# Performance work log

Hardware: AMD Instinct MI355X
Metric: run time of the kernel (lower is better)

The kernel has to match this reference:

```python
import jax, jax.numpy as jnp
import numpy as np

N_NODES = 131072
N_DST = 16384        # batch_size * num_supernodes = 8 * 2048
DEG = 16
N_EDGES = N_DST * DEG
IN_DIM, HID, NDIM = 3, 256, 2
POS_STD = 1.0


def _linear_params(key, fan_in, fan_out):
    # xavier_uniform weights, zero bias; torch Linear stores W as [out, in]
    limit = np.sqrt(6.0 / (fan_in + fan_out)).astype(np.float32)
    w = jax.random.uniform(key, (fan_out, fan_in), jnp.float32, -limit, limit)
    return w, jnp.zeros((fan_out,), jnp.float32)


def setup_inputs() -> dict:
    key = jax.random.key(0)
    ks = jax.random.split(key, 12)
    x = jax.random.normal(ks[0], (N_NODES, IN_DIM), jnp.float32)
    mesh_pos = jax.random.uniform(ks[1], (N_NODES, NDIM), jnp.float32)
    # dst column sorted, each supernode id 0..N_DST-1 appears DEG times (segment_csr layout)
    dst = jnp.repeat(jnp.arange(N_DST, dtype=jnp.int64), DEG)
    src = jax.random.randint(ks[2], (N_EDGES,), 0, N_NODES, jnp.int64)
    mesh_edges = jnp.stack([dst, src], axis=1)  # [E, 2] = (dst, src)
    batch_idx = jnp.repeat(jnp.arange(8, dtype=jnp.int64), N_NODES // 8)
    ip_w1, ip_b1 = _linear_params(ks[3], IN_DIM, HID)
    ip_w2, ip_b2 = _linear_params(ks[4], HID, HID)
    ip_w3, ip_b3 = _linear_params(ks[5], HID, HID)
    msg_w1, msg_b1 = _linear_params(ks[6], 2 * HID, 2 * HID)
    msg_w2, msg_b2 = _linear_params(ks[7], 2 * HID, HID)
    msg_w3, msg_b3 = _linear_params(ks[8], HID, HID)
    b_fourier = jax.random.normal(ks[9], (HID // 2, NDIM), jnp.float32) * POS_STD
    return {
        "x": x, "mesh_pos": mesh_pos, "mesh_edges": mesh_edges, "batch_idx": batch_idx,
        "ip_w1": ip_w1, "ip_b1": ip_b1, "ip_w2": ip_w2, "ip_b2": ip_b2,
        "ip_w3": ip_w3, "ip_b3": ip_b3, "b_fourier": b_fourier,
        "msg_w1": msg_w1, "msg_b1": msg_b1, "msg_w2": msg_w2, "msg_b2": msg_b2,
        "msg_w3": msg_w3, "msg_b3": msg_b3,
        "batch_size": 8, "num_supernodes": 2048,
    }


def reference(x, mesh_pos, mesh_edges, batch_idx,
              ip_w1, ip_b1, ip_w2, ip_b2, ip_w3, ip_b3, b_fourier,
              msg_w1, msg_b1, msg_w2, msg_b2, msg_w3, msg_b3,
              batch_size, num_supernodes):
    gelu = lambda t: jax.nn.gelu(t, approximate=False)  # torch nn.GELU default (erf)
    # input_proj MLP
    h = gelu(x @ ip_w1.T + ip_b1)
    h = gelu(h @ ip_w2.T + ip_b2)
    h = h @ ip_w3.T + ip_b3
    # gaussian sincos positional embedding
    proj = (2.0 * jnp.pi) * (mesh_pos @ b_fourier.T)  # [N, HID/2]
    h = h + jnp.concatenate([jnp.cos(proj), jnp.sin(proj)], axis=-1)
    # edge gather + concat + message MLP
    dst, src = mesh_edges[:, 0], mesh_edges[:, 1]
    m = jnp.concatenate([h[src], h[dst]], axis=1)  # [E, 2*HID]
    m = gelu(m @ msg_w1.T + msg_b1)
    m = gelu(m @ msg_w2.T + msg_b2)
    m = m @ msg_w3.T + msg_b3
    # segment mean over (sorted, compact) destination supernodes
    num_dst = batch_size * num_supernodes
    sums = jax.ops.segment_sum(m, dst, num_segments=num_dst)
    counts = jax.ops.segment_sum(jnp.ones((dst.shape[0],), m.dtype), dst, num_segments=num_dst)
    out = sums / jnp.maximum(counts, 1.0)[:, None]
    return out.reshape(batch_size, num_supernodes, out.shape[-1])
```

## Files before the change

### kernel.cpp

```cpp
#include <hip/hip_runtime.h>
#include <math.h>

#define N_NODES 131072
#define N_DST   16384
#define DEG     16
#define HID     256
#define N_EDGES 262144

typedef __bf16 bf16_8 __attribute__((ext_vector_type(8)));
typedef float  f32_4  __attribute__((ext_vector_type(4)));

__device__ __forceinline__ float gelu_f(float v) {
    float u = fmaf(v * v, -0.10294324f, -2.30220819f) * v;
    float e;
    asm("v_exp_f32 %0, %1" : "=v"(e) : "v"(u));
    return v * __builtin_amdgcn_rcpf(1.0f + e);
}
__device__ __forceinline__ f32_4 zero4() {
    f32_4 z; z[0] = 0.f; z[1] = 0.f; z[2] = 0.f; z[3] = 0.f; return z;
}

__device__ __forceinline__ void load_lds16(const __bf16* g, __bf16* l) {
    __builtin_amdgcn_global_load_lds(
        (__attribute__((address_space(1))) void*)g,
        (__attribute__((address_space(3))) void*)l, 16, 0, 0);
}

__global__ void prep_kernel(__bf16* __restrict__ out,
                            const float* __restrict__ w2,
                            const float* __restrict__ w3,
                            const float* __restrict__ mw1,
                            const float* __restrict__ mw2,
                            const float* __restrict__ mw3) {
    int stride = gridDim.x * blockDim.x;
    for (int i = blockIdx.x * blockDim.x + threadIdx.x; i < 589824; i += stride) {
        float v;
        if      (i <  65536) v = w2[i];
        else if (i < 131072) v = w3[i - 65536];
        else if (i < 393216) v = mw1[i - 131072];
        else if (i < 524288) v = mw2[i - 393216];
        else                 v = mw3[i - 524288];
        out[i] = (__bf16)v;
    }
}

__global__ __launch_bounds__(256) void enc1_kernel(
    const float* __restrict__ x, const float* __restrict__ w1,
    const float* __restrict__ b1, __bf16* __restrict__ h1) {
    const int c8   = threadIdx.x & 31;
    const int nloc = threadIdx.x >> 5;
    float w[24], bb[8];
    #pragma unroll
    for (int i = 0; i < 6; i++) *(float4*)&w[i * 4] = ((const float4*)w1)[c8 * 6 + i];
    *(float4*)&bb[0] = ((const float4*)b1)[c8 * 2 + 0];
    *(float4*)&bb[4] = ((const float4*)b1)[c8 * 2 + 1];
    for (int n = blockIdx.x * 8 + nloc; n < N_NODES; n += gridDim.x * 8) {
        float x0 = x[n * 3 + 0], x1 = x[n * 3 + 1], x2 = x[n * 3 + 2];
        bf16_8 o;
        #pragma unroll
        for (int j = 0; j < 8; j++) {
            float v = fmaf(x2, w[j * 3 + 2],
                      fmaf(x1, w[j * 3 + 1],
                      fmaf(x0, w[j * 3 + 0], bb[j])));
            o[j] = (__bf16)gelu_f(v);
        }
        *(bf16_8*)&h1[(size_t)n * 256 + c8 * 8] = o;
    }
}

__global__ __launch_bounds__(256, 2) void enc23_kernel(
    __bf16* __restrict__ hA,
    const __bf16* __restrict__ W2, const float* __restrict__ b2,
    const __bf16* __restrict__ W3, const float* __restrict__ b3,
    const float* __restrict__ pos, const float* __restrict__ bfour)
{
    __shared__ __align__(16) __bf16 sA[64 * 64];
    __shared__ __align__(16) __bf16 sB[16384];
    __shared__ __align__(16) __bf16 sH2[64 * 256];

    const int tid = threadIdx.x;
    const int m0  = blockIdx.x * 64;
    const int wave = tid >> 6, lane = tid & 63, ln = lane & 15, quad = lane >> 4;
    const int wm = wave >> 1, wn = wave & 1;

    const __bf16* pA[2];
    #pragma unroll
    for (int i = 0; i < 2; i++) {
        int idx = i * 256 + tid;
        int row = idx >> 3, kg = (idx & 7) ^ (row & 7);
        pA[i] = hA + (size_t)(m0 + row) * 256 + kg * 8;
    }

    f32_4 acc[2][8];
    #pragma unroll
    for (int i = 0; i < 2; i++)
        #pragma unroll
        for (int j = 0; j < 8; j++) acc[i][j] = zero4();

    bf16_8 ar[2];
    #pragma unroll
    for (int i = 0; i < 2; i++) ar[i] = *(const bf16_8*)pA[i];

    #pragma unroll
    for (int kb = 0; kb < 4; kb++) {
        if (kb > 0) __syncthreads();
        #pragma unroll
        for (int i = 0; i < 2; i++)
            *(bf16_8*)&sA[(i * 256 + tid) * 8] = ar[i];
        #pragma unroll
        for (int i = 0; i < 8; i++) {
            int idx = i * 256 + tid;
            int row = idx >> 3, kg = (idx & 7) ^ (row & 7);
            load_lds16(W2 + (size_t)row * 256 + kb * 64 + kg * 8, &sB[idx * 8]);
        }
        __syncthreads();
        if (kb < 3) {
            #pragma unroll
            for (int i = 0; i < 2; i++)
                ar[i] = *(const bf16_8*)(pA[i] + (kb + 1) * 64);
        }
        #pragma unroll
        for (int ks = 0; ks < 2; ks++) {
            int c = ks * 4 + quad;
            bf16_8 af[2], bfr[8];
            #pragma unroll
            for (int mt = 0; mt < 2; mt++) {
                int mr = wm * 32 + mt * 16 + ln;
                af[mt] = *(const bf16_8*)&sA[mr * 64 + (c ^ (mr & 7)) * 8];
            }
            #pragma unroll
            for (int nt = 0; nt < 8; nt++) {
                int nr = wn * 128 + nt * 16 + ln;
                bfr[nt] = *(const bf16_8*)&sB[nr * 64 + (c ^ (nr & 7)) * 8];
            }
            #pragma unroll
            for (int mt = 0; mt < 2; mt++)
                #pragma unroll
                for (int nt = 0; nt < 8; nt++)
                    acc[mt][nt] = __builtin_amdgcn_mfma_f32_16x16x32_bf16(af[mt], bfr[nt], acc[mt][nt], 0, 0, 0);
        }
    }
    #pragma unroll
    for (int nt = 0; nt < 8; nt++) {
        int col = wn * 128 + nt * 16 + ln;
        float bb = b2[col];
        #pragma unroll
        for (int mt = 0; mt < 2; mt++) {
            #pragma unroll
            for (int r = 0; r < 4; r++) {
                int row = wm * 32 + mt * 16 + quad * 4 + r;
                sH2[row * 256 + ((col + row * 8) & 255)] = (__bf16)gelu_f(acc[mt][nt][r] + bb);
            }
        }
    }
    #pragma unroll
    for (int i = 0; i < 2; i++)
        #pragma unroll
        for (int j = 0; j < 8; j++) acc[i][j] = zero4();
    __syncthreads();

    #pragma unroll
    for (int kb = 0; kb < 4; kb++) {
        if (kb > 0) __syncthreads();
        #pragma unroll
        for (int i = 0; i < 8; i++) {
            int idx = i * 256 + tid;
            int row = idx >> 3, kg = (idx & 7) ^ (row & 7);
            load_lds16(W3 + (size_t)row * 256 + kb * 64 + kg * 8, &sB[idx * 8]);
        }
        __syncthreads();
        #pragma unroll
        for (int ks = 0; ks < 2; ks++) {
            int c = ks * 4 + quad;
            int k0 = kb * 64 + ks * 32 + quad * 8;
            bf16_8 af[2], bfr[8];
            #pragma unroll
            for (int mt = 0; mt < 2; mt++) {
                int mr = wm * 32 + mt * 16 + ln;
                af[mt] = *(const bf16_8*)&sH2[mr * 256 + ((k0 + mr * 8) & 255)];
            }
            #pragma unroll
            for (int nt = 0; nt < 8; nt++) {
                int nr = wn * 128 + nt * 16 + ln;
                bfr[nt] = *(const bf16_8*)&sB[nr * 64 + (c ^ (nr & 7)) * 8];
            }
            #pragma unroll
            for (int mt = 0; mt < 2; mt++)
                #pragma unroll
                for (int nt = 0; nt < 8; nt++)
                    acc[mt][nt] = __builtin_amdgcn_mfma_f32_16x16x32_bf16(af[mt], bfr[nt], acc[mt][nt], 0, 0, 0);
        }
    }
    __syncthreads();
    __bf16* buf = sB + wave * 4096;
    float b3r[8], Bc0[8], Bc1[8];
    #pragma unroll
    for (int nt = 0; nt < 8; nt++) {
        int col = wn * 128 + nt * 16 + ln;
        b3r[nt] = b3[col];
        int jm = col & 127;
        Bc0[nt] = bfour[jm * 2 + 0];
        Bc1[nt] = bfour[jm * 2 + 1];
    }
    const bool iscos = (wn == 0);
    #pragma unroll
    for (int mt = 0; mt < 2; mt++) {
        #pragma unroll
        for (int r = 0; r < 4; r++) {
            int rowL = mt * 16 + quad * 4 + r;
            int rowE = m0 + wm * 32 + rowL;
            float p0 = pos[rowE * 2 + 0], p1 = pos[rowE * 2 + 1];
            #pragma unroll
            for (int nt = 0; nt < 8; nt++) {
                float f = 6.2831853071795864f * fmaf(p1, Bc1[nt], p0 * Bc0[nt]);
                float v = acc[mt][nt][r] + b3r[nt] + (iscos ? __cosf(f) : __sinf(f));
                int colL = nt * 16 + ln;
                buf[rowL * 128 + ((colL + rowL * 8) & 127)] = (__bf16)v;
            }
        }
    }
    #pragma unroll
    for (int p = 0; p < 8; p++) {
        int rowL = p * 4 + (lane >> 4);
        int c8 = lane & 15;
        bf16_8 vv = *(const bf16_8*)&buf[rowL * 128 + ((c8 * 8 + rowL * 8) & 127)];
        *(bf16_8*)&hA[(size_t)(m0 + wm * 32 + rowL) * 256 + wn * 128 + c8 * 8] = vv;
    }
}

__global__ __launch_bounds__(256, 2) void msg_fused(
    const __bf16* __restrict__ h, const int* __restrict__ edges,
    const __bf16* __restrict__ W1a, const float* __restrict__ b1,
    const __bf16* __restrict__ dmat, const __bf16* __restrict__ W2,
    const float* __restrict__ b2, __bf16* __restrict__ p2)
{
    __shared__ __align__(16) __bf16 sH[64 * 256];
    __shared__ __align__(16) __bf16 sB[16384];
    __shared__ __align__(16) __bf16 sM1[64 * 128];

    const int tid = threadIdx.x;
    const int e0  = blockIdx.x * 64;
    const int wave = tid >> 6, lane = tid & 63, ln = lane & 15, quad = lane >> 4;
    const int wm = wave >> 1, wn = wave & 1;

    int* s_src = (int*)sB;
    if (tid < 64) s_src[tid] = edges[2 * (e0 + tid) + 1];
    __syncthreads();

    const __bf16* pH[8];
    #pragma unroll
    for (int i = 0; i < 8; i++) {
        int idx = i * 256 + tid;
        int row = idx >> 5, kg = (idx & 31) ^ (row & 7);
        pH[i] = h + (size_t)s_src[row] * 256 + kg * 8;
    }
    __syncthreads();
    #pragma unroll
    for (int i = 0; i < 8; i++)
        load_lds16(pH[i], &sH[(i * 256 + tid) * 8]);

    f32_4 acc2[2][8];
    #pragma unroll
    for (int i = 0; i < 2; i++)
        #pragma unroll
        for (int j = 0; j < 8; j++) acc2[i][j] = zero4();

    #pragma unroll 1
    for (int q = 0; q < 4; q++) {
        const int colbase = q * 128 + wn * 64;
        float b1r[4];
        float dr[2][4];
        #pragma unroll
        for (int nt = 0; nt < 4; nt++) {
            b1r[nt] = b1[colbase + nt * 16 + ln];
            #pragma unroll
            for (int mt = 0; mt < 2; mt++) {
                int gid = blockIdx.x * 4 + wm * 2 + mt;
                dr[mt][nt] = (float)dmat[(size_t)gid * 512 + colbase + nt * 16 + ln];
            }
        }
        f32_4 acc1[2][4];
        #pragma unroll
        for (int i = 0; i < 2; i++)
            #pragma unroll
            for (int j = 0; j < 4; j++) acc1[i][j] = zero4();

        #pragma unroll
        for (int kb = 0; kb < 2; kb++) {
            __syncthreads();
            #pragma unroll
            for (int i = 0; i < 8; i++) {
                int idx = i * 256 + tid;
                int row = idx >> 4, kg = (idx & 15) ^ (row & 7);
                load_lds16(W1a + (size_t)(q * 128 + row) * 512 + kb * 128 + kg * 8,
                           &sB[idx * 8]);
            }
            __syncthreads();
            #pragma unroll
            for (int ks = 0; ks < 4; ks++) {
                int ca = kb * 16 + ks * 4 + quad;
                int cb = ks * 4 + quad;
                bf16_8 af[2], bfr[4];
                #pragma unroll
                for (int mt = 0; mt < 2; mt++) {
                    int mr = wm * 32 + mt * 16 + ln;
                    af[mt] = *(const bf16_8*)&sH[mr * 256 + (ca ^ (mr & 7)) * 8];
                }
                #pragma unroll
                for (int nt = 0; nt < 4; nt++) {
                    int nr = wn * 64 + nt * 16 + ln;
                    bfr[nt] = *(const bf16_8*)&sB[nr * 128 + (cb ^ (nr & 7)) * 8];
                }
                #pragma unroll
                for (int mt = 0; mt < 2; mt++)
                    #pragma unroll
                    for (int nt = 0; nt < 4; nt++)
                        acc1[mt][nt] = __builtin_amdgcn_mfma_f32_16x16x32_bf16(af[mt], bfr[nt], acc1[mt][nt], 0, 0, 0);
            }
        }
        #pragma unroll
        for (int mt = 0; mt < 2; mt++) {
            #pragma unroll
            for (int nt = 0; nt < 4; nt++) {
                #pragma unroll
                for (int r = 0; r < 4; r++) {
                    int row = wm * 32 + mt * 16 + quad * 4 + r;
                    int colq = wn * 64 + nt * 16 + ln;
                    float v = gelu_f(acc1[mt][nt][r] + b1r[nt] + dr[mt][nt]);
                    sM1[row * 128 + ((colq + row * 8) & 127)] = (__bf16)v;
                }
            }
        }
        __syncthreads();

        #pragma unroll
        for (int kb2 = 0; kb2 < 2; kb2++) {
            if (kb2 > 0) __syncthreads();
            #pragma unroll
            for (int i = 0; i < 8; i++) {
                int idx = i * 256 + tid;
                int row = idx >> 3, kg = (idx & 7) ^ (row & 7);
                load_lds16(W2 + (size_t)row * 512 + q * 128 + kb2 * 64 + kg * 8,
                           &sB[idx * 8]);
            }
            __syncthreads();
            #pragma unroll
            for (int ks = 0; ks < 2; ks++) {
                int k0 = kb2 * 64 + ks * 32 + quad * 8;
                int cb2 = ks * 4 + quad;
                bf16_8 af[2], bfr[8];
                #pragma unroll
                for (int mt = 0; mt < 2; mt++) {
                    int mr = wm * 32 + mt * 16 + ln;
                    af[mt] = *(const bf16_8*)&sM1[mr * 128 + ((k0 + mr * 8) & 127)];
                }
                #pragma unroll
                for (int nt = 0; nt < 8; nt++) {
                    int nr = wn * 128 + nt * 16 + ln;
                    bfr[nt] = *(const bf16_8*)&sB[nr * 64 + (cb2 ^ (nr & 7)) * 8];
                }
                #pragma unroll
                for (int mt = 0; mt < 2; mt++)
                    #pragma unroll
                    for (int nt = 0; nt < 8; nt++)
                        acc2[mt][nt] = __builtin_amdgcn_mfma_f32_16x16x32_bf16(af[mt], bfr[nt], acc2[mt][nt], 0, 0, 0);
            }
        }
        __syncthreads();
    }

    #pragma unroll
    for (int nt = 0; nt < 8; nt++) {
        int col = wn * 128 + nt * 16 + ln;
        float bb = b2[col];
        #pragma unroll
        for (int mt = 0; mt < 2; mt++) {
            float s = gelu_f(acc2[mt][nt][0] + bb) + gelu_f(acc2[mt][nt][1] + bb)
                    + gelu_f(acc2[mt][nt][2] + bb) + gelu_f(acc2[mt][nt][3] + bb);
            s += __shfl_xor(s, 16);
            s += __shfl_xor(s, 32);
            if (quad == 0) {
                int dstn = edges[2 * (e0 + (wm * 2 + mt) * 16)];
                p2[(size_t)dstn * HID + col] = (__bf16)(s * 0.0625f);
            }
        }
    }
}

template<int K, int GMODE, int WLD, int WOFF, bool BIAS, bool POOL_, bool F32OUT>
__global__ __launch_bounds__(256, 3) void mgemm(
    const __bf16* __restrict__ Ag, const __bf16* __restrict__ h,
    const int* __restrict__ edges, const __bf16* __restrict__ W,
    const float* __restrict__ bias, __bf16* __restrict__ Cb,
    float* __restrict__ Cf, int NB, int Nfull, int e0)
{
    __shared__ __align__(16) __bf16 sA[128 * 64];
    __shared__ __align__(16) __bf16 sB[128 * 64];
    __shared__ int s_idx[128];

    const int tid  = threadIdx.x;
    const int mblk = blockIdx.x / NB;
    const int nblk = blockIdx.x % NB;
    const int m0 = mblk * 128, n0 = nblk * 128;
    const int wave = tid >> 6, lane = tid & 63, ln = lane & 15, quad = lane >> 4;
    const int wm = wave >> 1, wn = wave & 1;

    if (GMODE) {
        if (tid < 128) {
            int r = m0 + tid;
            s_idx[tid] = (GMODE == 1) ? edges[2 * (e0 + r) + 1]
                                      : edges[2 * (DEG * r)];
        }
        __syncthreads();
    }

    const __bf16* pA[4];
    const __bf16* pB[4];
    #pragma unroll
    for (int i = 0; i < 4; i++) {
        int idx = i * 256 + tid;
        int row = idx >> 3, kg = (idx & 7) ^ (row & 7);
        pA[i] = GMODE ? h + (size_t)s_idx[row] * HID + kg * 8
                      : Ag + (size_t)(m0 + row) * K + kg * 8;
        pB[i] = W + (size_t)(n0 + row) * WLD + WOFF + kg * 8;
    }
    const int ach = quad ^ (ln & 7);
    const int aof[2] = { (wm * 64 + ln) * 64 + ach * 8, (wm * 64 + ln) * 64 + (ach ^ 4) * 8 };
    const int bof[2] = { (wn * 64 + ln) * 64 + ach * 8, (wn * 64 + ln) * 64 + (ach ^ 4) * 8 };

    f32_4 acc[4][4];
    #pragma unroll
    for (int i = 0; i < 4; i++)
        #pragma unroll
        for (int j = 0; j < 4; j++) acc[i][j] = zero4();

    bf16_8 ar[4], br[4];
    #pragma unroll
    for (int i = 0; i < 4; i++) {
        ar[i] = *(const bf16_8*)pA[i];
        br[i] = *(const bf16_8*)pB[i];
    }

    #pragma unroll
    for (int kb = 0; kb < K / 64; kb++) {
        if (kb > 0) __syncthreads();
        #pragma unroll
        for (int i = 0; i < 4; i++) {
            int idx = i * 256 + tid;
            *(bf16_8*)&sA[idx * 8] = ar[i];
            *(bf16_8*)&sB[idx * 8] = br[i];
        }
        __syncthreads();
        if (kb + 1 < K / 64) {
            #pragma unroll
            for (int i = 0; i < 4; i++) {
                ar[i] = *(const bf16_8*)(pA[i] + (kb + 1) * 64);
                br[i] = *(const bf16_8*)(pB[i] + (kb + 1) * 64);
            }
        }
        #pragma unroll
        for (int ks = 0; ks < 2; ks++) {
            bf16_8 af[4], bfr[4];
            #pragma unroll
            for (int mt = 0; mt < 4; mt++) af[mt]  = *(const bf16_8*)&sA[aof[ks] + mt * 1024];
            #pragma unroll
            for (int nt = 0; nt < 4; nt++) bfr[nt] = *(const bf16_8*)&sB[bof[ks] + nt * 1024];
            #pragma unroll
            for (int mt = 0; mt < 4; mt++)
                #pragma unroll
                for (int nt = 0; nt < 4; nt++)
                    acc[mt][nt] = __builtin_amdgcn_mfma_f32_16x16x32_bf16(af[mt], bfr[nt], acc[mt][nt], 0, 0, 0);
        }
    }

    if (POOL_) {
        #pragma unroll
        for (int nt = 0; nt < 4; nt++) {
            int col = n0 + wn * 64 + nt * 16 + ln;
            float bb = BIAS ? bias[col] : 0.f;
            #pragma unroll
            for (int mt = 0; mt < 4; mt++) {
                float s = gelu_f(acc[mt][nt][0] + bb) + gelu_f(acc[mt][nt][1] + bb)
                        + gelu_f(acc[mt][nt][2] + bb) + gelu_f(acc[mt][nt][3] + bb);
                s += __shfl_xor(s, 16);
                s += __shfl_xor(s, 32);
                if (quad == 0) {
                    int eg  = e0 + m0 + wm * 64 + mt * 16;
                    int dstn = edges[2 * eg];
                    Cb[(size_t)dstn * HID + col] = (__bf16)(s * 0.0625f);
                }
            }
        }
    } else if (F32OUT) {
        #pragma unroll
        for (int nt = 0; nt < 4; nt++) {
            int col = n0 + wn * 64 + nt * 16 + ln;
            float bb = BIAS ? bias[col] : 0.f;
            #pragma unroll
            for (int mt = 0; mt < 4; mt++) {
                #pragma unroll
                for (int r = 0; r < 4; r++) {
                    int rowE = m0 + wm * 64 + mt * 16 + quad * 4 + r;
                    Cf[(size_t)rowE * Nfull + col] = acc[mt][nt][r] + bb;
                }
            }
        }
    } else {
        __syncthreads();
        __bf16* sw = ((wave & 2) ? sB : sA) + (wave & 1) * 4096;
        #pragma unroll
        for (int nt = 0; nt < 4; nt++) {
            #pragma unroll
            for (int mt = 0; mt < 4; mt++) {
                #pragma unroll
                for (int r = 0; r < 4; r++) {
                    int rowL = mt * 16 + quad * 4 + r;
                    int colL = nt * 16 + ln;
                    sw[rowL * 64 + ((colL + rowL * 8) & 63)] = (__bf16)acc[mt][nt][r];
                }
            }
        }
        __syncthreads();
        #pragma unroll
        for (int p = 0; p < 8; p++) {
            int rowL = p * 8 + (lane >> 3);
            int c8 = lane & 7;
            bf16_8 vv = *(const bf16_8*)&sw[rowL * 64 + ((c8 * 8 + rowL * 8) & 63)];
            int rowE = m0 + wm * 64 + rowL;
            *(bf16_8*)&Cb[(size_t)rowE * Nfull + n0 + wn * 64 + c8 * 8] = vv;
        }
    }
}

extern "C" void kernel_launch(void* const* d_in, const int* in_sizes, int n_in,
                              void* d_out, int out_size, void* d_ws, size_t ws_size,
                              hipStream_t stream) {
    const float* x     = (const float*)d_in[0];
    const float* pos   = (const float*)d_in[1];
    const int*   edges = (const int*)d_in[2];
    const float* ip_w1 = (const float*)d_in[4];
    const float* ip_b1 = (const float*)d_in[5];
    const float* ip_w2 = (const float*)d_in[6];
    const float* ip_b2 = (const float*)d_in[7];
    const float* ip_w3 = (const float*)d_in[8];
    const float* ip_b3 = (const float*)d_in[9];
    const float* bfour = (const float*)d_in[10];
    const float* mw1   = (const float*)d_in[11];
    const float* mb1   = (const float*)d_in[12];
    const float* mw2   = (const float*)d_in[13];
    const float* mb2   = (const float*)d_in[14];
    const float* mw3   = (const float*)d_in[15];
    const float* mb3   = (const float*)d_in[16];

    char* ws = (char*)d_ws;
    __bf16* hA = (__bf16*)ws;
    size_t off = (size_t)N_NODES * HID * 2;
    __bf16* wb = (__bf16*)(ws + off);
    off += (size_t)589824 * 2;
    off = (off + 255) & ~(size_t)255;
    __bf16* dbuf = (__bf16*)(ws + off);
    off += (size_t)N_DST * 512 * 2;
    __bf16* p2 = (__bf16*)(ws + off);
    off += (size_t)N_DST * HID * 2;

    __bf16* w2b  = wb;
    __bf16* w3b  = wb + 65536;
    __bf16* mw1b = wb + 131072;
    __bf16* mw2b = wb + 393216;
    __bf16* mw3b = wb + 524288;

    prep_kernel<<<2304, 256, 0, stream>>>(wb, ip_w2, ip_w3, mw1, mw2, mw3);

    enc1_kernel<<<2048, 256, 0, stream>>>(x, ip_w1, ip_b1, hA);
    enc23_kernel<<<2048, 256, 0, stream>>>(hA, w2b, ip_b2, w3b, ip_b3, pos, bfour);

    mgemm<256, 2, 512, 256, false, false, false><<<512, 256, 0, stream>>>(
        nullptr, hA, edges, mw1b, nullptr, dbuf, nullptr, 4, 512, 0);

    msg_fused<<<4096, 256, 0, stream>>>(hA, edges, mw1b, mb1, dbuf, mw2b, mb2, p2);

    mgemm<256, 0, 256, 0, true, false, true><<<256, 256, 0, stream>>>(
        p2, nullptr, nullptr, mw3b, mb3, nullptr, (float*)d_out, 2, 256, 0);
}
```

Baseline: 438.6 us.

## Double-buffer weight tiles, keep gathered rows in registers, use 128-edge blocks

msg_fused now runs 512 threads per block over 128 edges, so each loaded weight tile serves twice as many rows. The gathered h rows go straight from global memory into per-wave registers instead of through LDS. Weight tiles are double-buffered in LDS, with the next tile's async load issued before the current tile's MFMAs, so load latency overlaps compute and fewer barriers are needed. The cost is higher register pressure (64 extra VGPRs per thread for the A fragments), which under launch_bounds(512,2) may cause spills or lower occupancy.

```diff
diff --git a/kernel.cpp b/kernel.cpp
--- a/kernel.cpp
+++ b/kernel.cpp
@@ -228,54 +228,73 @@
     }
 }
 
-__global__ __launch_bounds__(256, 2) void msg_fused(
+__global__ __launch_bounds__(512, 2) void msg_fused(
     const __bf16* __restrict__ h, const int* __restrict__ edges,
     const __bf16* __restrict__ W1a, const float* __restrict__ b1,
     const __bf16* __restrict__ dmat, const __bf16* __restrict__ W2,
     const float* __restrict__ b2, __bf16* __restrict__ p2)
 {
-    __shared__ __align__(16) __bf16 sH[64 * 256];
-    __shared__ __align__(16) __bf16 sB[16384];
-    __shared__ __align__(16) __bf16 sM1[64 * 128];
+    __shared__ __align__(16) __bf16 sB[2][16384];
+    __shared__ __align__(16) __bf16 sM1[16384];
 
     const int tid = threadIdx.x;
-    const int e0  = blockIdx.x * 64;
+    const int e0  = blockIdx.x * 128;
     const int wave = tid >> 6, lane = tid & 63, ln = lane & 15, quad = lane >> 4;
     const int wm = wave >> 1, wn = wave & 1;
 
-    int* s_src = (int*)sB;
-    if (tid < 64) s_src[tid] = edges[2 * (e0 + tid) + 1];
+    bf16_8 aA[2][8];
+    #pragma unroll
+    for (int mt = 0; mt < 2; mt++) {
+        int row = wm * 32 + mt * 16 + ln;
+        int src = edges[2 * (e0 + row) + 1];
+        const __bf16* base = h + (size_t)src * 256 + quad * 8;
+        #pragma unroll
+        for (int c = 0; c < 8; c++)
+            aA[mt][c] = *(const bf16_8*)(base + c * 32);
+    }
+
+    int w1e[4], w2e[4];
+    #pragma unroll
+    for (int i = 0; i < 4; i++) {
+        int idx = i * 512 + tid;
+        int r1 = idx >> 4, k1 = (idx & 15) ^ (r1 & 7);
+        w1e[i] = r1 * 512 + k1 * 8;
+        int r2 = idx >> 3, k2 = (idx & 7) ^ (r2 & 7);
+        w2e[i] = r2 * 512 + k2 * 8;
+    }
+
+    auto stage_w1 = [&](int q, int kb, int p) {
+        const __bf16* srcb = W1a + (size_t)q * 128 * 512 + kb * 128;
+        #pragma unroll
+        for (int i = 0; i < 4; i++)
+            load_lds16(srcb + w1e[i], &sB[p][(i * 512 + tid) * 8]);
+    };
+    auto stage_w2 = [&](int q, int kb2, int p) {
+        const __bf16* srcb = W2 + q * 128 + kb2 * 64;
+        #pragma unroll
+        for (int i = 0; i < 4; i++)
+            load_lds16(srcb + w2e[i], &sB[p][(i * 512 + tid) * 8]);
+    };
+
+    f32_4 acc2[2][8];
+    #pragma unroll
+    for (int i = 0; i < 2; i++)
+        #pragma unroll
+        for (int j = 0; j < 8; j++) acc2[i][j] = zero4();
+
+    stage_w1(0, 0, 0);
     __syncthreads();
-
-    const __bf16* pH[8];
-    #pragma unroll
-    for (int i = 0; i < 8; i++) {
-        int idx = i * 256 + tid;
-        int row = idx >> 5, kg = (idx & 31) ^ (row & 7);
-        pH[i] = h + (size_t)s_src[row] * 256 + kg * 8;
-    }
-    __syncthreads();
-    #pragma unroll
-    for (int i = 0; i < 8; i++)
-        load_lds16(pH[i], &sH[(i * 256 + tid) * 8]);
-
-    f32_4 acc2[2][8];
-    #pragma unroll
-    for (int i = 0; i < 2; i++)
-        #pragma unroll
-        for (int j = 0; j < 8; j++) acc2[i][j] = zero4();
 
     #pragma unroll 1
     for (int q = 0; q < 4; q++) {
         const int colbase = q * 128 + wn * 64;
-        float b1r[4];
-        float dr[2][4];
+        float b1r[4], dr[2][4];
         #pragma unroll
         for (int nt = 0; nt < 4; nt++) {
             b1r[nt] = b1[colbase + nt * 16 + ln];
             #pragma unroll
             for (int mt = 0; mt < 2; mt++) {
-                int gid = blockIdx.x * 4 + wm * 2 + mt;
+                int gid = blockIdx.x * 8 + wm * 2 + mt;
                 dr[mt][nt] = (float)dmat[(size_t)gid * 512 + colbase + nt * 16 + ln];
             }
         }
@@ -285,38 +304,37 @@
             #pragma unroll
             for (int j = 0; j < 4; j++) acc1[i][j] = zero4();
 
-        #pragma unroll
-        for (int kb = 0; kb < 2; kb++) {
-            __syncthreads();
-            #pragma unroll
-            for (int i = 0; i < 8; i++) {
-                int idx = i * 256 + tid;
-                int row = idx >> 4, kg = (idx & 15) ^ (row & 7);
-                load_lds16(W1a + (size_t)(q * 128 + row) * 512 + kb * 128 + kg * 8,
-                           &sB[idx * 8]);
-            }
-            __syncthreads();
-            #pragma unroll
-            for (int ks = 0; ks < 4; ks++) {
-                int ca = kb * 16 + ks * 4 + quad;
-                int cb = ks * 4 + quad;
-                bf16_8 af[2], bfr[4];
-                #pragma unroll
-                for (int mt = 0; mt < 2; mt++) {
-                    int mr = wm * 32 + mt * 16 + ln;
-                    af[mt] = *(const bf16_8*)&sH[mr * 256 + (ca ^ (mr & 7)) * 8];
-                }
-                #pragma unroll
-                for (int nt = 0; nt < 4; nt++) {
-                    int nr = wn * 64 + nt * 16 + ln;
-                    bfr[nt] = *(const bf16_8*)&sB[nr * 128 + (cb ^ (nr & 7)) * 8];
-                }
-                #pragma unroll
-                for (int mt = 0; mt < 2; mt++)
-                    #pragma unroll
-                    for (int nt = 0; nt < 4; nt++)
-                        acc1[mt][nt] = __builtin_amdgcn_mfma_f32_16x16x32_bf16(af[mt], bfr[nt], acc1[mt][nt], 0, 0, 0);
-            }
+        stage_w1(q, 1, 1);
+        #pragma unroll
+        for (int ks = 0; ks < 4; ks++) {
+            bf16_8 bfr[4];
+            #pragma unroll
+            for (int nt = 0; nt < 4; nt++) {
+                int nr = wn * 64 + nt * 16 + ln;
+                bfr[nt] = *(const bf16_8*)&sB[0][nr * 128 + (((ks * 4 + quad) ^ (nr & 7)) * 8)];
+            }
+            #pragma unroll
+            for (int mt = 0; mt < 2; mt++)
+                #pragma unroll
+                for (int nt = 0; nt < 4; nt++)
+                    acc1[mt][nt] = __builtin_amdgcn_mfma_f32_16x16x32_bf16(aA[mt][ks], bfr[nt], acc1[mt][nt], 0, 0, 0);
+        }
+        __syncthreads();
+
+        stage_w2(q, 0, 0);
+        #pragma unroll
+        for (int ks = 0; ks < 4; ks++) {
+            bf16_8 bfr[4];
+            #pragma unroll
+            for (int nt = 0; nt < 4; nt++) {
+                int nr = wn * 64 + nt * 16 + ln;
+                bfr[nt] = *(const bf16_8*)&sB[1][nr * 128 + (((ks * 4 + quad) ^ (nr & 7)) * 8)];
+            }
+            #pragma unroll
+            for (int mt = 0; mt < 2; mt++)
+                #pragma unroll
+                for (int nt = 0; nt < 4; nt++)
+                    acc1[mt][nt] = __builtin_amdgcn_mfma_f32_16x16x32_bf16(aA[mt][4 + ks], bfr[nt], acc1[mt][nt], 0, 0, 0);
         }
         #pragma unroll
         for (int mt = 0; mt < 2; mt++) {
@@ -333,38 +351,49 @@
         }
         __syncthreads();
 
-        #pragma unroll
-        for (int kb2 = 0; kb2 < 2; kb2++) {
-            if (kb2 > 0) __syncthreads();
-            #pragma unroll
-            for (int i = 0; i < 8; i++) {
-                int idx = i * 256 + tid;
-                int row = idx >> 3, kg = (idx & 7) ^ (row & 7);
-                load_lds16(W2 + (size_t)row * 512 + q * 128 + kb2 * 64 + kg * 8,
-                           &sB[idx * 8]);
-            }
-            __syncthreads();
-            #pragma unroll
-            for (int ks = 0; ks < 2; ks++) {
-                int k0 = kb2 * 64 + ks * 32 + quad * 8;
-                int cb2 = ks * 4 + quad;
-                bf16_8 af[2], bfr[8];
-                #pragma unroll
-                for (int mt = 0; mt < 2; mt++) {
-                    int mr = wm * 32 + mt * 16 + ln;
-                    af[mt] = *(const bf16_8*)&sM1[mr * 128 + ((k0 + mr * 8) & 127)];
-                }
-                #pragma unroll
-                for (int nt = 0; nt < 8; nt++) {
-                    int nr = wn * 128 + nt * 16 + ln;
-                    bfr[nt] = *(const bf16_8*)&sB[nr * 64 + (cb2 ^ (nr & 7)) * 8];
-                }
-                #pragma unroll
-                for (int mt = 0; mt < 2; mt++)
-                    #pragma unroll
-                    for (int nt = 0; nt < 8; nt++)
-                        acc2[mt][nt] = __builtin_amdgcn_mfma_f32_16x16x32_bf16(af[mt], bfr[nt], acc2[mt][nt], 0, 0, 0);
-            }
+        stage_w2(q, 1, 1);
+        #pragma unroll
+        for (int ks = 0; ks < 2; ks++) {
+            int k0 = ks * 32 + quad * 8;
+            bf16_8 af[2], bfr[8];
+            #pragma unroll
+            for (int mt = 0; mt < 2; mt++) {
+                int mr = wm * 32 + mt * 16 + ln;
+                af[mt] = *(const bf16_8*)&sM1[mr * 128 + ((k0 + mr * 8) & 127)];
+            }
+            #pragma unroll
+            for (int nt = 0; nt < 8; nt++) {
+                int nr = wn * 128 + nt * 16 + ln;
+                bfr[nt] = *(const bf16_8*)&sB[0][nr * 64 + (((ks * 4 + quad) ^ (nr & 7)) * 8)];
+            }
+            #pragma unroll
+            for (int mt = 0; mt < 2; mt++)
+                #pragma unroll
+                for (int nt = 0; nt < 8; nt++)
+                    acc2[mt][nt] = __builtin_amdgcn_mfma_f32_16x16x32_bf16(af[mt], bfr[nt], acc2[mt][nt], 0, 0, 0);
+        }
+        __syncthreads();
+
+        if (q < 3) stage_w1(q + 1, 0, 0);
+        #pragma unroll
+        for (int ks = 0; ks < 2; ks++) {
+            int k0 = 64 + ks * 32 + quad * 8;
+            bf16_8 af[2], bfr[8];
+            #pragma unroll
+            for (int mt = 0; mt < 2; mt++) {
+                int mr = wm * 32 + mt * 16 + ln;
+                af[mt] = *(const bf16_8*)&sM1[mr * 128 + ((k0 + mr * 8) & 127)];
+            }
+            #pragma unroll
+            for (int nt = 0; nt < 8; nt++) {
+                int nr = wn * 128 + nt * 16 + ln;
+                bfr[nt] = *(const bf16_8*)&sB[1][nr * 64 + (((ks * 4 + quad) ^ (nr & 7)) * 8)];
+            }
+            #pragma unroll
+            for (int mt = 0; mt < 2; mt++)
+                #pragma unroll
+                for (int nt = 0; nt < 8; nt++)
+                    acc2[mt][nt] = __builtin_amdgcn_mfma_f32_16x16x32_bf16(af[mt], bfr[nt], acc2[mt][nt], 0, 0, 0);
         }
         __syncthreads();
     }
@@ -577,7 +606,7 @@
     mgemm<256, 2, 512, 256, false, false, false><<<512, 256, 0, stream>>>(
         nullptr, hA, edges, mw1b, nullptr, dbuf, nullptr, 4, 512, 0);
 
-    msg_fused<<<4096, 256, 0, stream>>>(hA, edges, mw1b, mb1, dbuf, mw2b, mb2, p2);
+    msg_fused<<<2048, 512, 0, stream>>>(hA, edges, mw1b, mb1, dbuf, mw2b, mb2, p2);
 
     mgemm<256, 0, 256, 0, true, false, true><<<256, 256, 0, stream>>>(
         p2, nullptr, nullptr, mw3b, mb3, nullptr, (float*)d_out, 2, 256, 0);
```

New measurement: 448.7 us. 1.02x slower.

## Precompute per-node first message-layer projection and gather it per edge

Applied to the files above, without the earlier changes.

The source half of the first message linear layer is now computed once per node by a separate GEMM into a new 512-wide bf16 buffer. The fused message kernel gathers those projected rows per edge, adds the per-destination term, and applies GELU before the second layer. The first-layer bias moves into the destination GEMM epilogue. This halves the first-layer matrix FLOPs and frees LDS so the kernel can run at occupancy 3, but it writes a large node-level intermediate and doubles the bytes gathered per edge.

```diff
diff --git a/kernel.cpp b/kernel.cpp
--- a/kernel.cpp
+++ b/kernel.cpp
@@ -228,37 +228,23 @@
     }
 }
 
-__global__ __launch_bounds__(256, 2) void msg_fused(
-    const __bf16* __restrict__ h, const int* __restrict__ edges,
-    const __bf16* __restrict__ W1a, const float* __restrict__ b1,
+__global__ __launch_bounds__(256, 3) void msg_fused(
+    const __bf16* __restrict__ an, const int* __restrict__ edges,
     const __bf16* __restrict__ dmat, const __bf16* __restrict__ W2,
     const float* __restrict__ b2, __bf16* __restrict__ p2)
 {
-    __shared__ __align__(16) __bf16 sH[64 * 256];
+    __shared__ __align__(16) __bf16 sM1[8192];
     __shared__ __align__(16) __bf16 sB[16384];
-    __shared__ __align__(16) __bf16 sM1[64 * 128];
+    __shared__ int s_src[64];
 
     const int tid = threadIdx.x;
     const int e0  = blockIdx.x * 64;
     const int wave = tid >> 6, lane = tid & 63, ln = lane & 15, quad = lane >> 4;
     const int wm = wave >> 1, wn = wave & 1;
 
-    int* s_src = (int*)sB;
     if (tid < 64) s_src[tid] = edges[2 * (e0 + tid) + 1];
     __syncthreads();
 
-    const __bf16* pH[8];
-    #pragma unroll
-    for (int i = 0; i < 8; i++) {
-        int idx = i * 256 + tid;
-        int row = idx >> 5, kg = (idx & 31) ^ (row & 7);
-        pH[i] = h + (size_t)s_src[row] * 256 + kg * 8;
-    }
-    __syncthreads();
-    #pragma unroll
-    for (int i = 0; i < 8; i++)
-        load_lds16(pH[i], &sH[(i * 256 + tid) * 8]);
-
     f32_4 acc2[2][8];
     #pragma unroll
     for (int i = 0; i < 2; i++)
@@ -267,75 +253,31 @@
 
     #pragma unroll 1
     for (int q = 0; q < 4; q++) {
-        const int colbase = q * 128 + wn * 64;
-        float b1r[4];
-        float dr[2][4];
-        #pragma unroll
-        for (int nt = 0; nt < 4; nt++) {
-            b1r[nt] = b1[colbase + nt * 16 + ln];
-            #pragma unroll
-            for (int mt = 0; mt < 2; mt++) {
-                int gid = blockIdx.x * 4 + wm * 2 + mt;
-                dr[mt][nt] = (float)dmat[(size_t)gid * 512 + colbase + nt * 16 + ln];
-            }
-        }
-        f32_4 acc1[2][4];
-        #pragma unroll
-        for (int i = 0; i < 2; i++)
-            #pragma unroll
-            for (int j = 0; j < 4; j++) acc1[i][j] = zero4();
-
-        #pragma unroll
-        for (int kb = 0; kb < 2; kb++) {
-            __syncthreads();
-            #pragma unroll
-            for (int i = 0; i < 8; i++) {
-                int idx = i * 256 + tid;
-                int row = idx >> 4, kg = (idx & 15) ^ (row & 7);
-                load_lds16(W1a + (size_t)(q * 128 + row) * 512 + kb * 128 + kg * 8,
-                           &sB[idx * 8]);
-            }
-            __syncthreads();
-            #pragma unroll
-            for (int ks = 0; ks < 4; ks++) {
-                int ca = kb * 16 + ks * 4 + quad;
-                int cb = ks * 4 + quad;
-                bf16_8 af[2], bfr[4];
-                #pragma unroll
-                for (int mt = 0; mt < 2; mt++) {
-                    int mr = wm * 32 + mt * 16 + ln;
-                    af[mt] = *(const bf16_8*)&sH[mr * 256 + (ca ^ (mr & 7)) * 8];
-                }
-                #pragma unroll
-                for (int nt = 0; nt < 4; nt++) {
-                    int nr = wn * 64 + nt * 16 + ln;
-                    bfr[nt] = *(const bf16_8*)&sB[nr * 128 + (cb ^ (nr & 7)) * 8];
-                }
-                #pragma unroll
-                for (int mt = 0; mt < 2; mt++)
-                    #pragma unroll
-                    for (int nt = 0; nt < 4; nt++)
-                        acc1[mt][nt] = __builtin_amdgcn_mfma_f32_16x16x32_bf16(af[mt], bfr[nt], acc1[mt][nt], 0, 0, 0);
-            }
-        }
-        #pragma unroll
-        for (int mt = 0; mt < 2; mt++) {
-            #pragma unroll
-            for (int nt = 0; nt < 4; nt++) {
-                #pragma unroll
-                for (int r = 0; r < 4; r++) {
-                    int row = wm * 32 + mt * 16 + quad * 4 + r;
-                    int colq = wn * 64 + nt * 16 + ln;
-                    float v = gelu_f(acc1[mt][nt][r] + b1r[nt] + dr[mt][nt]);
-                    sM1[row * 128 + ((colq + row * 8) & 127)] = (__bf16)v;
-                }
-            }
-        }
-        __syncthreads();
+        #pragma unroll
+        for (int i = 0; i < 4; i++) {
+            int idx = i * 256 + tid;
+            int row = idx >> 4, kgl = idx & 15, kg = kgl ^ (row & 7);
+            load_lds16(an + (size_t)s_src[row] * 512 + q * 128 + kg * 8,
+                       &sM1[idx * 8]);
+        }
+        __syncthreads();
+
+        #pragma unroll
+        for (int i = 0; i < 4; i++) {
+            int idx = i * 256 + tid;
+            int row = idx >> 4, kgl = idx & 15, kg = kgl ^ (row & 7);
+            int gid = blockIdx.x * 4 + (row >> 4);
+            bf16_8 a = *(const bf16_8*)&sM1[idx * 8];
+            bf16_8 d = *(const bf16_8*)&dmat[(size_t)gid * 512 + q * 128 + kg * 8];
+            bf16_8 o;
+            #pragma unroll
+            for (int j = 0; j < 8; j++)
+                o[j] = (__bf16)gelu_f((float)a[j] + (float)d[j]);
+            *(bf16_8*)&sM1[idx * 8] = o;
+        }
 
         #pragma unroll
         for (int kb2 = 0; kb2 < 2; kb2++) {
-            if (kb2 > 0) __syncthreads();
             #pragma unroll
             for (int i = 0; i < 8; i++) {
                 int idx = i * 256 + tid;
@@ -346,18 +288,18 @@
             __syncthreads();
             #pragma unroll
             for (int ks = 0; ks < 2; ks++) {
-                int k0 = kb2 * 64 + ks * 32 + quad * 8;
+                int c2  = kb2 * 8 + ks * 4 + quad;
                 int cb2 = ks * 4 + quad;
                 bf16_8 af[2], bfr[8];
                 #pragma unroll
                 for (int mt = 0; mt < 2; mt++) {
                     int mr = wm * 32 + mt * 16 + ln;
-                    af[mt] = *(const bf16_8*)&sM1[mr * 128 + ((k0 + mr * 8) & 127)];
+                    af[mt] = *(const bf16_8*)&sM1[mr * 128 + ((c2 ^ (mr & 7)) * 8)];
                 }
                 #pragma unroll
                 for (int nt = 0; nt < 8; nt++) {
                     int nr = wn * 128 + nt * 16 + ln;
-                    bfr[nt] = *(const bf16_8*)&sB[nr * 64 + (cb2 ^ (nr & 7)) * 8];
+                    bfr[nt] = *(const bf16_8*)&sB[nr * 64 + ((cb2 ^ (nr & 7)) * 8)];
                 }
                 #pragma unroll
                 for (int mt = 0; mt < 2; mt++)
@@ -365,8 +307,8 @@
                     for (int nt = 0; nt < 8; nt++)
                         acc2[mt][nt] = __builtin_amdgcn_mfma_f32_16x16x32_bf16(af[mt], bfr[nt], acc2[mt][nt], 0, 0, 0);
             }
-        }
-        __syncthreads();
+            __syncthreads();
+        }
     }
 
     #pragma unroll
@@ -510,13 +452,14 @@
         __bf16* sw = ((wave & 2) ? sB : sA) + (wave & 1) * 4096;
         #pragma unroll
         for (int nt = 0; nt < 4; nt++) {
+            float bb = BIAS ? bias[n0 + wn * 64 + nt * 16 + ln] : 0.f;
             #pragma unroll
             for (int mt = 0; mt < 4; mt++) {
                 #pragma unroll
                 for (int r = 0; r < 4; r++) {
                     int rowL = mt * 16 + quad * 4 + r;
                     int colL = nt * 16 + ln;
-                    sw[rowL * 64 + ((colL + rowL * 8) & 63)] = (__bf16)acc[mt][nt][r];
+                    sw[rowL * 64 + ((colL + rowL * 8) & 63)] = (__bf16)(acc[mt][nt][r] + bb);
                 }
             }
         }
@@ -558,6 +501,8 @@
     __bf16* wb = (__bf16*)(ws + off);
     off += (size_t)589824 * 2;
     off = (off + 255) & ~(size_t)255;
+    __bf16* anodes = (__bf16*)(ws + off);
+    off += (size_t)N_NODES * 512 * 2;
     __bf16* dbuf = (__bf16*)(ws + off);
     off += (size_t)N_DST * 512 * 2;
     __bf16* p2 = (__bf16*)(ws + off);
@@ -574,10 +519,13 @@
     enc1_kernel<<<2048, 256, 0, stream>>>(x, ip_w1, ip_b1, hA);
     enc23_kernel<<<2048, 256, 0, stream>>>(hA, w2b, ip_b2, w3b, ip_b3, pos, bfour);
 
-    mgemm<256, 2, 512, 256, false, false, false><<<512, 256, 0, stream>>>(
-        nullptr, hA, edges, mw1b, nullptr, dbuf, nullptr, 4, 512, 0);
-
-    msg_fused<<<4096, 256, 0, stream>>>(hA, edges, mw1b, mb1, dbuf, mw2b, mb2, p2);
+    mgemm<256, 0, 512, 0, false, false, false><<<4096, 256, 0, stream>>>(
+        hA, nullptr, nullptr, mw1b, nullptr, anodes, nullptr, 4, 512, 0);
+
+    mgemm<256, 2, 512, 256, true, false, false><<<512, 256, 0, stream>>>(
+        nullptr, hA, edges, mw1b, mb1, dbuf, nullptr, 4, 512, 0);
+
+    msg_fused<<<4096, 256, 0, stream>>>(anodes, edges, dbuf, mw2b, mb2, p2);
 
     mgemm<256, 0, 256, 0, true, false, true><<<256, 256, 0, stream>>>(
         p2, nullptr, nullptr, mw3b, mb3, nullptr, (float*)d_out, 2, 256, 0);
```

Result: slower. 477.9 us (+9.0%).
